# Optimization experiments

Measured on AMD Instinct MI355X. Metric: run time of the kernel, lower is better.

The kernel has to match this reference:

```python
import jax, jax.numpy as jnp
import numpy as np
import math

B, S, E, H = 2, 2048, 1024, 16
D = E // H  # head dim = 64


def setup_inputs() -> dict:
    key = jax.random.key(0)
    ks = jax.random.split(key, 7)
    scale = 1.0 / math.sqrt(E)
    return {
        "query": jax.random.normal(ks[0], (B, S, E), dtype=jnp.float32),
        "key": jax.random.normal(ks[1], (B, S, E), dtype=jnp.float32),
        "value": jax.random.normal(ks[2], (B, S, E), dtype=jnp.float32),
        # packed in-projection: (3E, E) weights, (3E,) bias, q/k/v order
        "in_proj_weight": jax.random.normal(ks[3], (3 * E, E), dtype=jnp.float32) * scale,
        "in_proj_bias": jnp.zeros((3 * E,), dtype=jnp.float32),
        "out_proj_weight": jax.random.normal(ks[4], (E, E), dtype=jnp.float32) * scale,
        "out_proj_bias": jnp.zeros((E,), dtype=jnp.float32),
    }


def reference(query, key, value, in_proj_weight, in_proj_bias, out_proj_weight, out_proj_bias):
    # packed in-projection (q, k, v order), F.linear convention: x @ W^T + b
    w_q, w_k, w_v = jnp.split(in_proj_weight, 3, axis=0)
    b_q, b_k, b_v = jnp.split(in_proj_bias, 3, axis=0)
    q = query @ w_q.T + b_q   # [B, S, E]
    k = key @ w_k.T + b_k
    v = value @ w_v.T + b_v

    # split heads: [B, S, E] -> [B, H, S, D]
    def heads(x):
        return x.reshape(B, S, H, D).transpose(0, 2, 1, 3)

    q, k, v = heads(q), heads(k), heads(v)
    q = q / jnp.asarray(math.sqrt(D), dtype=q.dtype)

    # naive softmax attention (materializes [B, H, S, S] as original bmm+softmax+bmm)
    scores = jnp.einsum("bhqd,bhkd->bhqk", q, k)
    attn = jax.nn.softmax(scores, axis=-1)
    out = jnp.einsum("bhqk,bhkd->bhqd", attn, v)  # [B, H, S, D]

    out = out.transpose(0, 2, 1, 3).reshape(B, S, E)
    return out @ out_proj_weight.T + out_proj_bias
```

## Files before the change

### kernel.cpp

```cpp
#include <hip/hip_runtime.h>
#include <stdint.h>

#define LOG2E 1.44269504088896340736f

typedef __bf16 bf16x8 __attribute__((ext_vector_type(8)));
typedef float f32x4 __attribute__((ext_vector_type(4)));
typedef float f32x16 __attribute__((ext_vector_type(16)));

static constexpr int Bb = 2, Ss = 2048, Ee = 1024, Hh = 16, Dd = 64;
static constexpr int BSE = Bb * Ss * Ee;

static constexpr size_t OFF_QB    = 0;
static constexpr size_t OFF_KB    = 4194304;
static constexpr size_t OFF_VB    = 8388608;
static constexpr size_t OFF_WQKV  = 12582912;
static constexpr size_t OFF_WOUT  = 15728640;
static constexpr size_t OFF_QH    = 16777216;
static constexpr size_t OFF_KH    = 20971520;
static constexpr size_t OFF_VH    = 25165824;
static constexpr size_t OFF_OB    = 29360128;

__device__ __forceinline__ uint16_t f32_bf16(float f) {
    uint32_t u = __builtin_bit_cast(uint32_t, f);
    u += 0x7fffu + ((u >> 16) & 1u);
    return (uint16_t)(u >> 16);
}

__device__ __forceinline__ uint32_t cvt_pk_bf16(float a, float b) {
    uint32_t r;
    asm("v_cvt_pk_bf16_f32 %0, %1, %2" : "=v"(r) : "v"(a), "v"(b));
    return r;
}

__device__ __forceinline__ void perm32swap(uint32_t& x, uint32_t& y) {
    asm("v_permlane32_swap_b32 %0, %1" : "+v"(x), "+v"(y));
}

__global__ __launch_bounds__(256) void cvt_kernel(
    const float* __restrict__ q, const float* __restrict__ k, const float* __restrict__ v,
    const float* __restrict__ w1, uint16_t* __restrict__ ws)
{
    const float* srcs[4] = {q, k, v, w1};
    const int ns4[4] = {BSE/4, BSE/4, BSE/4, (3*Ee*Ee)/4};
    uint16_t* dsts[4] = {ws+OFF_QB, ws+OFF_KB, ws+OFF_VB, ws+OFF_WQKV};
    int z = blockIdx.z;
    int i = blockIdx.x * blockDim.x + threadIdx.x;
    if (i < ns4[z]) {
        float4 f = ((const float4*)srcs[z])[i];
        ushort4 o;
        o.x = f32_bf16(f.x); o.y = f32_bf16(f.y);
        o.z = f32_bf16(f.z); o.w = f32_bf16(f.w);
        ((ushort4*)dsts[z])[i] = o;
    }
}

__global__ __launch_bounds__(256) void cvt_one(
    const float* __restrict__ src, uint16_t* __restrict__ dst)
{
    int i = blockIdx.x * 256 + threadIdx.x;
    float4 f = ((const float4*)src)[i];
    ushort4 o;
    o.x = f32_bf16(f.x); o.y = f32_bf16(f.y);
    o.z = f32_bf16(f.z); o.w = f32_bf16(f.w);
    ((ushort4*)dst)[i] = o;
}

template<int MODE>
__global__ __launch_bounds__(256) void gemm_nt(
    const uint16_t* __restrict__ Aq, const uint16_t* __restrict__ Ak,
    const uint16_t* __restrict__ Av, const uint16_t* __restrict__ Bw,
    const float* __restrict__ bias, uint16_t* __restrict__ OutB,
    float* __restrict__ OutF)
{
    constexpr int K = Ee, N = Ee;
    const int tid = threadIdx.x;
    const int l = tid & 63, w = tid >> 6;
    const int wr = w >> 1, wc = w & 1;
    const int tm = blockIdx.y, tn = blockIdx.x;
    const int z = (MODE == 0) ? blockIdx.z : 0;

    const uint16_t* A = (MODE == 0) ? (z == 0 ? Aq : (z == 1 ? Ak : Av)) : Aq;
    const uint16_t* Bp = Bw + (size_t)z * Ee * Ee;
    const float* bp = bias + (size_t)z * Ee;

    __shared__ alignas(16) uint16_t As[128 * 32];
    __shared__ alignas(16) uint16_t Bs[128 * 32];

    f32x4 acc[4][4] = {};
    const int arow = tm * 128;
    const int bcol = tn * 128;

    for (int kt = 0; kt < K / 32; ++kt) {
        __syncthreads();
        #pragma unroll
        for (int it = 0; it < 2; ++it) {
            int c = tid + it * 256;
            int row = c >> 2, qq = c & 3;
            const uint16_t* ga = A  + (size_t)(arow + row) * K + kt * 32 + qq * 8;
            const uint16_t* gb = Bp + (size_t)(bcol + row) * K + kt * 32 + qq * 8;
            __builtin_amdgcn_global_load_lds(
                (const __attribute__((address_space(1))) void*)ga,
                (__attribute__((address_space(3))) void*)(As + c * 8), 16, 0, 0);
            __builtin_amdgcn_global_load_lds(
                (const __attribute__((address_space(1))) void*)gb,
                (__attribute__((address_space(3))) void*)(Bs + c * 8), 16, 0, 0);
        }
        __syncthreads();
        bf16x8 aF[4], bF[4];
        #pragma unroll
        for (int m = 0; m < 4; ++m)
            aF[m] = *(const bf16x8*)(As + ((wr * 64 + m * 16 + (l & 15)) * 32 + (l >> 4) * 8));
        #pragma unroll
        for (int n = 0; n < 4; ++n)
            bF[n] = *(const bf16x8*)(Bs + ((wc * 64 + n * 16 + (l & 15)) * 32 + (l >> 4) * 8));
        #pragma unroll
        for (int m = 0; m < 4; ++m)
            #pragma unroll
            for (int n = 0; n < 4; ++n)
                acc[m][n] = __builtin_amdgcn_mfma_f32_16x16x32_bf16(aF[m], bF[n], acc[m][n], 0, 0, 0);
    }

    #pragma unroll
    for (int n = 0; n < 4; ++n) {
        int col = bcol + wc * 64 + n * 16 + (l & 15);
        float bn = bp[col];
        #pragma unroll
        for (int m = 0; m < 4; ++m) {
            int row0 = arow + wr * 64 + m * 16 + (l >> 4) * 4;
            #pragma unroll
            for (int j = 0; j < 4; ++j) {
                int row = row0 + j;
                float v = acc[m][n][j] + bn;
                if (MODE == 0) {
                    if (z == 0) v *= 0.125f * LOG2E;
                    int b = row >> 11, s = row & 2047, hh = col >> 6, d = col & 63;
                    OutB[(size_t)z * BSE + (size_t)(((b * Hh) + hh) * Ss + s) * Dd + d] = f32_bf16(v);
                } else {
                    OutF[(size_t)row * N + col] = v;
                }
            }
        }
    }
}

__global__ __launch_bounds__(256, 3) void attn_kernel(
    const uint16_t* __restrict__ Qh, const uint16_t* __restrict__ Kh,
    const uint16_t* __restrict__ Vh, float* __restrict__ po,
    float* __restrict__ lpart)
{
    const int tid = threadIdx.x;
    const int l = tid & 63, w = tid >> 6;
    const int q = l & 31, hi = l >> 5;

    const int orig = blockIdx.x;
    const int L = (orig & 7) * 128 + (orig >> 3);
    const int qb = L & 15, split = (L >> 4) & 1, bh = L >> 5;

    const int q0 = qb * 128;
    const int keyb = split * 1024;
    const size_t base = (size_t)bh * Ss * Dd;

    __shared__ alignas(16) uint16_t Ks[2][64 * 64];
    __shared__ alignas(16) uint16_t Vt[2][64 * 64];

    bf16x8 qf[4];
    {
        const uint16_t* qp = Qh + base + (size_t)(q0 + w * 32 + q) * Dd + hi * 8;
        #pragma unroll
        for (int m = 0; m < 4; ++m) qf[m] = *(const bf16x8*)(qp + 16 * m);
    }

    const int kp = tid >> 3, c8v = tid & 7;
    uint4 vg0, vg1;

    auto loadK_lds = [&](int key0, int buf) {
        #pragma unroll
        for (int it = 0; it < 2; ++it) {
            int c = tid + 256 * it, row = c >> 3, cc = c & 7;
            const uint16_t* gk = Kh + base + (size_t)(key0 + row) * Dd + ((cc ^ (row & 7)) * 8);
            __builtin_amdgcn_global_load_lds(
                (const __attribute__((address_space(1))) void*)gk,
                (__attribute__((address_space(3))) void*)(&Ks[buf][c * 8]), 16, 0, 0);
        }
    };
    auto loadV = [&](int key0) {
        vg0 = *(const uint4*)(Vh + base + (size_t)(key0 + 2 * kp) * Dd + c8v * 8);
        vg1 = *(const uint4*)(Vh + base + (size_t)(key0 + 2 * kp + 1) * Dd + c8v * 8);
    };

    loadK_lds(keyb, 0);
    loadV(keyb);

    f32x16 o0 = {}, o1 = {};
    float lsum = 0.f;

    auto build_pb = [&](const f32x16& sv, bf16x8* pbout) {
        uint32_t W[4][2];
        #pragma unroll
        for (int a = 0; a < 4; ++a) {
            float p0 = __builtin_amdgcn_exp2f(sv[4 * a + 0]);
            float p1 = __builtin_amdgcn_exp2f(sv[4 * a + 1]);
            float p2 = __builtin_amdgcn_exp2f(sv[4 * a + 2]);
            float p3 = __builtin_amdgcn_exp2f(sv[4 * a + 3]);
            lsum += (p0 + p1) + (p2 + p3);
            W[a][0] = cvt_pk_bf16(p0, p1);
            W[a][1] = cvt_pk_bf16(p2, p3);
        }
        #pragma unroll
        for (int kl = 0; kl < 2; ++kl) {
            uint32_t x0 = W[2 * kl][0], x1 = W[2 * kl][1];
            uint32_t y0 = W[2 * kl + 1][0], y1 = W[2 * kl + 1][1];
            perm32swap(x0, y0);
            perm32swap(x1, y1);
            union { uint32_t u[4]; bf16x8 v; } pu;
            pu.u[0] = x0; pu.u[1] = x1; pu.u[2] = y0; pu.u[3] = y1;
            pbout[kl] = pu.v;
        }
    };

    #pragma unroll 2
    for (int kt = 0; kt < 16; ++kt) {
        const int b = kt & 1;
        __syncthreads();

        {
            const uint16_t* e0 = (const uint16_t*)&vg0;
            const uint16_t* e1 = (const uint16_t*)&vg1;
            #pragma unroll
            for (int e = 0; e < 8; ++e) {
                int d = c8v * 8 + e;
                int swz = (kp >> 2) ^ e ^ c8v;
                uint32_t pk2 = (uint32_t)e0[e] | ((uint32_t)e1[e] << 16);
                *(uint32_t*)&Vt[b][d * 64 + swz * 8 + ((2 * kp) & 7)] = pk2;
            }
        }

        if (kt < 15) {
            loadK_lds(keyb + (kt + 1) * 64, b ^ 1);
            loadV(keyb + (kt + 1) * 64);
        }

        __syncthreads();

        f32x16 s0 = {}, s1 = {};
        __builtin_amdgcn_s_setprio(1);
        #pragma unroll
        for (int m = 0; m < 4; ++m) {
            int sw = ((2 * m + hi) ^ (q & 7)) << 3;
            bf16x8 k0 = *(const bf16x8*)&Ks[b][q * 64 + sw];
            bf16x8 k1 = *(const bf16x8*)&Ks[b][(32 + q) * 64 + sw];
            s0 = __builtin_amdgcn_mfma_f32_32x32x16_bf16(k0, qf[m], s0, 0, 0, 0);
            s1 = __builtin_amdgcn_mfma_f32_32x32x16_bf16(k1, qf[m], s1, 0, 0, 0);
        }
        __builtin_amdgcn_s_setprio(0);

        bf16x8 pb[4];
        build_pb(s0, pb + 0);
        build_pb(s1, pb + 2);

        __builtin_amdgcn_s_setprio(1);
        #pragma unroll
        for (int ka = 0; ka < 4; ++ka) {
            #pragma unroll
            for (int dt = 0; dt < 2; ++dt) {
                int d = 32 * dt + q;
                int swz = (2 * ka + hi) ^ (d & 7) ^ (d >> 3);
                bf16x8 vf = *(const bf16x8*)&Vt[b][d * 64 + swz * 8];
                if (dt == 0)
                    o0 = __builtin_amdgcn_mfma_f32_32x32x16_bf16(vf, pb[ka], o0, 0, 0, 0);
                else
                    o1 = __builtin_amdgcn_mfma_f32_32x32x16_bf16(vf, pb[ka], o1, 0, 0, 0);
            }
        }
        __builtin_amdgcn_s_setprio(0);
    }

    float lr = lsum + __shfl_xor(lsum, 32);
    const int qrow = q0 + w * 32 + q;
    const int sb = split * 32 + bh;
    if (hi == 0) lpart[(size_t)sb * 2048 + qrow] = lr;
    #pragma unroll
    for (int dt = 0; dt < 2; ++dt) {
        const f32x16& oo = dt ? o1 : o0;
        #pragma unroll
        for (int rr = 0; rr < 16; ++rr) {
            int d = 32 * dt + (rr & 3) + 8 * (rr >> 2) + 4 * hi;
            po[((size_t)sb * 64 + d) * 2048 + qrow] = oo[rr];
        }
    }
}

__global__ __launch_bounds__(256) void combine_kernel(
    const float* __restrict__ po, const float* __restrict__ lp,
    uint16_t* __restrict__ Ob)
{
    __shared__ float T[64][65];
    const int t = threadIdx.x;
    const int bh = blockIdx.y;
    const int q0 = blockIdx.x * 64;
    const int qq = t & 63;
    const float inv = 1.0f / (lp[bh * 2048 + q0 + qq] + lp[(32 + bh) * 2048 + q0 + qq]);
    const size_t b0 = (size_t)bh * 64 * 2048;
    const size_t b1 = (size_t)(32 + bh) * 64 * 2048;
    #pragma unroll
    for (int i = 0; i < 16; ++i) {
        int d = i * 4 + (t >> 6);
        size_t off = (size_t)d * 2048 + q0 + qq;
        T[d][qq] = (po[b0 + off] + po[b1 + off]) * inv;
    }
    __syncthreads();
    const int row = t >> 2, dc = (t & 3) * 16;
    const int bb = bh >> 4, hh = bh & 15;
    union { uint16_t u[16]; uint4 v[2]; } pk;
    #pragma unroll
    for (int e = 0; e < 16; ++e) pk.u[e] = f32_bf16(T[dc + e][row]);
    uint16_t* dst = &Ob[(size_t)(bb * 2048 + q0 + row) * 1024 + hh * 64 + dc];
    *(uint4*)dst = pk.v[0];
    *((uint4*)dst + 1) = pk.v[1];
}

extern "C" void kernel_launch(void* const* d_in, const int* in_sizes, int n_in,
                              void* d_out, int out_size, void* d_ws, size_t ws_size,
                              hipStream_t stream) {
    (void)in_sizes; (void)n_in; (void)out_size; (void)ws_size;
    const float* query = (const float*)d_in[0];
    const float* key   = (const float*)d_in[1];
    const float* value = (const float*)d_in[2];
    const float* w_in  = (const float*)d_in[3];
    const float* b_in  = (const float*)d_in[4];
    const float* w_out = (const float*)d_in[5];
    const float* b_out = (const float*)d_in[6];
    uint16_t* ws = (uint16_t*)d_ws;

    uint16_t* qb    = ws + OFF_QB;
    uint16_t* kb    = ws + OFF_KB;
    uint16_t* vb    = ws + OFF_VB;
    uint16_t* wqkvb = ws + OFF_WQKV;
    uint16_t* woutb = ws + OFF_WOUT;
    uint16_t* Qh    = ws + OFF_QH;
    uint16_t* Kh    = ws + OFF_KH;
    uint16_t* Vh    = ws + OFF_VH;
    uint16_t* Ob    = ws + OFF_OB;
    float*    po    = (float*)d_ws;
    float*    lpart = (float*)d_out;

    cvt_kernel<<<dim3(4096, 1, 4), 256, 0, stream>>>(query, key, value, w_in, ws);
    gemm_nt<0><<<dim3(8, 32, 3), 256, 0, stream>>>(qb, kb, vb, wqkvb, b_in, Qh, nullptr);
    attn_kernel<<<dim3(1024), 256, 0, stream>>>(Qh, Kh, Vh, po, lpart);
    combine_kernel<<<dim3(32, 32), 256, 0, stream>>>(po, lpart, Ob);
    cvt_one<<<dim3(1024), 256, 0, stream>>>(w_out, woutb);
    gemm_nt<1><<<dim3(8, 32, 1), 256, 0, stream>>>(Ob, nullptr, nullptr, woutb, b_out, nullptr, (float*)d_out);
}
```

Before: 138.3 us.

## Emit V transposed from projection GEMM and process two query tiles per attention block

The V projection is computed as W_v·V^T, so the GEMM writes V directly in a [bh, d, s] transposed layout. The attention kernel can then stage V into LDS with async global_load_lds instead of loading it through registers and transposing it in software. This also drops one barrier per iteration. Each attention block now covers 256 queries (two 128-row sets sharing every K/V tile), halving the grid and the K/V traffic per query, at the cost of more registers and lower occupancy (launch bound 2).

```diff
diff --git a/kernel.cpp b/kernel.cpp
--- a/kernel.cpp
+++ b/kernel.cpp
@@ -76,11 +76,13 @@
     const int tid = threadIdx.x;
     const int l = tid & 63, w = tid >> 6;
     const int wr = w >> 1, wc = w & 1;
-    const int tm = blockIdx.y, tn = blockIdx.x;
     const int z = (MODE == 0) ? blockIdx.z : 0;
-
-    const uint16_t* A = (MODE == 0) ? (z == 0 ? Aq : (z == 1 ? Ak : Av)) : Aq;
-    const uint16_t* Bp = Bw + (size_t)z * Ee * Ee;
+    const bool VT = (MODE == 0) && (z == 2);
+    const int tm = VT ? blockIdx.x : blockIdx.y;
+    const int tn = VT ? blockIdx.y : blockIdx.x;
+
+    const uint16_t* A = (MODE == 0) ? (z == 0 ? Aq : (z == 1 ? Ak : Bw + 2 * Ee * Ee)) : Aq;
+    const uint16_t* Bp = VT ? Av : (Bw + (size_t)z * Ee * Ee);
     const float* bp = bias + (size_t)z * Ee;
 
     __shared__ alignas(16) uint16_t As[128 * 32];
@@ -123,29 +125,35 @@
     #pragma unroll
     for (int n = 0; n < 4; ++n) {
         int col = bcol + wc * 64 + n * 16 + (l & 15);
-        float bn = bp[col];
+        float bn = VT ? 0.f : bp[col];
         #pragma unroll
         for (int m = 0; m < 4; ++m) {
             int row0 = arow + wr * 64 + m * 16 + (l >> 4) * 4;
             #pragma unroll
             for (int j = 0; j < 4; ++j) {
                 int row = row0 + j;
-                float v = acc[m][n][j] + bn;
                 if (MODE == 0) {
-                    if (z == 0) v *= 0.125f * LOG2E;
-                    int b = row >> 11, s = row & 2047, hh = col >> 6, d = col & 63;
-                    OutB[(size_t)z * BSE + (size_t)(((b * Hh) + hh) * Ss + s) * Dd + d] = f32_bf16(v);
+                    if (VT) {
+                        float v = acc[m][n][j] + bp[row];
+                        int hh = row >> 6, d = row & 63, b = col >> 11, s = col & 2047;
+                        OutB[2 * (size_t)BSE + ((size_t)((b * Hh + hh) * Dd + d)) * Ss + s] = f32_bf16(v);
+                    } else {
+                        float v = acc[m][n][j] + bn;
+                        if (z == 0) v *= 0.125f * LOG2E;
+                        int b = row >> 11, s = row & 2047, hh = col >> 6, d = col & 63;
+                        OutB[(size_t)z * BSE + (size_t)(((b * Hh) + hh) * Ss + s) * Dd + d] = f32_bf16(v);
+                    }
                 } else {
-                    OutF[(size_t)row * N + col] = v;
+                    OutF[(size_t)row * N + col] = acc[m][n][j] + bn;
                 }
             }
         }
     }
 }
 
-__global__ __launch_bounds__(256, 3) void attn_kernel(
+__global__ __launch_bounds__(256, 2) void attn_kernel(
     const uint16_t* __restrict__ Qh, const uint16_t* __restrict__ Kh,
-    const uint16_t* __restrict__ Vh, float* __restrict__ po,
+    const uint16_t* __restrict__ Vtg, float* __restrict__ po,
     float* __restrict__ lpart)
 {
     const int tid = threadIdx.x;
@@ -153,48 +161,53 @@
     const int q = l & 31, hi = l >> 5;
 
     const int orig = blockIdx.x;
-    const int L = (orig & 7) * 128 + (orig >> 3);
-    const int qb = L & 15, split = (L >> 4) & 1, bh = L >> 5;
-
-    const int q0 = qb * 128;
+    const int L = (orig & 7) * 64 + (orig >> 3);
+    const int qb = L & 7, split = (L >> 3) & 1, bh = L >> 4;
+
+    const int q0 = qb * 256;
     const int keyb = split * 1024;
-    const size_t base = (size_t)bh * Ss * Dd;
+    const size_t baseK = (size_t)bh * Ss * Dd;
+    const size_t baseV = (size_t)bh * Dd * Ss;
 
     __shared__ alignas(16) uint16_t Ks[2][64 * 64];
     __shared__ alignas(16) uint16_t Vt[2][64 * 64];
 
-    bf16x8 qf[4];
+    bf16x8 qfA[4], qfB[4];
     {
-        const uint16_t* qp = Qh + base + (size_t)(q0 + w * 32 + q) * Dd + hi * 8;
-        #pragma unroll
-        for (int m = 0; m < 4; ++m) qf[m] = *(const bf16x8*)(qp + 16 * m);
-    }
-
-    const int kp = tid >> 3, c8v = tid & 7;
-    uint4 vg0, vg1;
-
-    auto loadK_lds = [&](int key0, int buf) {
+        const uint16_t* qp = Qh + baseK + (size_t)(q0 + w * 32 + q) * Dd + hi * 8;
+        #pragma unroll
+        for (int m = 0; m < 4; ++m) {
+            qfA[m] = *(const bf16x8*)(qp + 16 * m);
+            qfB[m] = *(const bf16x8*)(qp + 128 * Dd + 16 * m);
+        }
+    }
+
+    auto stage = [&](int kt, int buf) {
+        const int key0 = keyb + kt * 64;
         #pragma unroll
         for (int it = 0; it < 2; ++it) {
             int c = tid + 256 * it, row = c >> 3, cc = c & 7;
-            const uint16_t* gk = Kh + base + (size_t)(key0 + row) * Dd + ((cc ^ (row & 7)) * 8);
+            const uint16_t* gk = Kh + baseK + (size_t)(key0 + row) * Dd + ((cc ^ (row & 7)) * 8);
             __builtin_amdgcn_global_load_lds(
                 (const __attribute__((address_space(1))) void*)gk,
                 (__attribute__((address_space(3))) void*)(&Ks[buf][c * 8]), 16, 0, 0);
         }
+        #pragma unroll
+        for (int it = 0; it < 2; ++it) {
+            int c = tid + 256 * it, d = c >> 3, j = c & 7;
+            const uint16_t* gv = Vtg + baseV + (size_t)d * Ss + key0 + 8 * (j ^ (d & 7) ^ (d >> 3));
+            __builtin_amdgcn_global_load_lds(
+                (const __attribute__((address_space(1))) void*)gv,
+                (__attribute__((address_space(3))) void*)(&Vt[buf][c * 8]), 16, 0, 0);
+        }
     };
-    auto loadV = [&](int key0) {
-        vg0 = *(const uint4*)(Vh + base + (size_t)(key0 + 2 * kp) * Dd + c8v * 8);
-        vg1 = *(const uint4*)(Vh + base + (size_t)(key0 + 2 * kp + 1) * Dd + c8v * 8);
-    };
-
-    loadK_lds(keyb, 0);
-    loadV(keyb);
-
-    f32x16 o0 = {}, o1 = {};
-    float lsum = 0.f;
-
-    auto build_pb = [&](const f32x16& sv, bf16x8* pbout) {
+
+    stage(0, 0);
+
+    f32x16 oA0 = {}, oA1 = {}, oB0 = {}, oB1 = {};
+    float lsumA = 0.f, lsumB = 0.f;
+
+    auto build_pb = [&](const f32x16& sv, bf16x8* pbout, float& lsum) {
         uint32_t W[4][2];
         #pragma unroll
         for (int a = 0; a < 4; ++a) {
@@ -223,69 +236,83 @@
         const int b = kt & 1;
         __syncthreads();
 
+        if (kt < 15) stage(kt + 1, b ^ 1);
+
         {
-            const uint16_t* e0 = (const uint16_t*)&vg0;
-            const uint16_t* e1 = (const uint16_t*)&vg1;
-            #pragma unroll
-            for (int e = 0; e < 8; ++e) {
-                int d = c8v * 8 + e;
-                int swz = (kp >> 2) ^ e ^ c8v;
-                uint32_t pk2 = (uint32_t)e0[e] | ((uint32_t)e1[e] << 16);
-                *(uint32_t*)&Vt[b][d * 64 + swz * 8 + ((2 * kp) & 7)] = pk2;
+            f32x16 s0 = {}, s1 = {};
+            __builtin_amdgcn_s_setprio(1);
+            #pragma unroll
+            for (int m = 0; m < 4; ++m) {
+                int sw = ((2 * m + hi) ^ (q & 7)) << 3;
+                bf16x8 k0 = *(const bf16x8*)&Ks[b][q * 64 + sw];
+                bf16x8 k1 = *(const bf16x8*)&Ks[b][(32 + q) * 64 + sw];
+                s0 = __builtin_amdgcn_mfma_f32_32x32x16_bf16(k0, qfA[m], s0, 0, 0, 0);
+                s1 = __builtin_amdgcn_mfma_f32_32x32x16_bf16(k1, qfA[m], s1, 0, 0, 0);
             }
-        }
-
-        if (kt < 15) {
-            loadK_lds(keyb + (kt + 1) * 64, b ^ 1);
-            loadV(keyb + (kt + 1) * 64);
-        }
-
-        __syncthreads();
-
-        f32x16 s0 = {}, s1 = {};
-        __builtin_amdgcn_s_setprio(1);
-        #pragma unroll
-        for (int m = 0; m < 4; ++m) {
-            int sw = ((2 * m + hi) ^ (q & 7)) << 3;
-            bf16x8 k0 = *(const bf16x8*)&Ks[b][q * 64 + sw];
-            bf16x8 k1 = *(const bf16x8*)&Ks[b][(32 + q) * 64 + sw];
-            s0 = __builtin_amdgcn_mfma_f32_32x32x16_bf16(k0, qf[m], s0, 0, 0, 0);
-            s1 = __builtin_amdgcn_mfma_f32_32x32x16_bf16(k1, qf[m], s1, 0, 0, 0);
-        }
-        __builtin_amdgcn_s_setprio(0);
-
-        bf16x8 pb[4];
-        build_pb(s0, pb + 0);
-        build_pb(s1, pb + 2);
-
-        __builtin_amdgcn_s_setprio(1);
-        #pragma unroll
-        for (int ka = 0; ka < 4; ++ka) {
-            #pragma unroll
-            for (int dt = 0; dt < 2; ++dt) {
-                int d = 32 * dt + q;
-                int swz = (2 * ka + hi) ^ (d & 7) ^ (d >> 3);
-                bf16x8 vf = *(const bf16x8*)&Vt[b][d * 64 + swz * 8];
-                if (dt == 0)
-                    o0 = __builtin_amdgcn_mfma_f32_32x32x16_bf16(vf, pb[ka], o0, 0, 0, 0);
-                else
-                    o1 = __builtin_amdgcn_mfma_f32_32x32x16_bf16(vf, pb[ka], o1, 0, 0, 0);
+            __builtin_amdgcn_s_setprio(0);
+            bf16x8 pb[4];
+            build_pb(s0, pb + 0, lsumA);
+            build_pb(s1, pb + 2, lsumA);
+            __builtin_amdgcn_s_setprio(1);
+            #pragma unroll
+            for (int ka = 0; ka < 4; ++ka)
+                #pragma unroll
+                for (int dt = 0; dt < 2; ++dt) {
+                    int d = 32 * dt + q;
+                    int swz = (2 * ka + hi) ^ (d & 7) ^ (d >> 3);
+                    bf16x8 vf = *(const bf16x8*)&Vt[b][d * 64 + swz * 8];
+                    if (dt == 0) oA0 = __builtin_amdgcn_mfma_f32_32x32x16_bf16(vf, pb[ka], oA0, 0, 0, 0);
+                    else         oA1 = __builtin_amdgcn_mfma_f32_32x32x16_bf16(vf, pb[ka], oA1, 0, 0, 0);
+                }
+            __builtin_amdgcn_s_setprio(0);
+        }
+        {
+            f32x16 s0 = {}, s1 = {};
+            __builtin_amdgcn_s_setprio(1);
+            #pragma unroll
+            for (int m = 0; m < 4; ++m) {
+                int sw = ((2 * m + hi) ^ (q & 7)) << 3;
+                bf16x8 k0 = *(const bf16x8*)&Ks[b][q * 64 + sw];
+                bf16x8 k1 = *(const bf16x8*)&Ks[b][(32 + q) * 64 + sw];
+                s0 = __builtin_amdgcn_mfma_f32_32x32x16_bf16(k0, qfB[m], s0, 0, 0, 0);
+                s1 = __builtin_amdgcn_mfma_f32_32x32x16_bf16(k1, qfB[m], s1, 0, 0, 0);
             }
-        }
-        __builtin_amdgcn_s_setprio(0);
-    }
-
-    float lr = lsum + __shfl_xor(lsum, 32);
-    const int qrow = q0 + w * 32 + q;
+            __builtin_amdgcn_s_setprio(0);
+            bf16x8 pb[4];
+            build_pb(s0, pb + 0, lsumB);
+            build_pb(s1, pb + 2, lsumB);
+            __builtin_amdgcn_s_setprio(1);
+            #pragma unroll
+            for (int ka = 0; ka < 4; ++ka)
+                #pragma unroll
+                for (int dt = 0; dt < 2; ++dt) {
+                    int d = 32 * dt + q;
+                    int swz = (2 * ka + hi) ^ (d & 7) ^ (d >> 3);
+                    bf16x8 vf = *(const bf16x8*)&Vt[b][d * 64 + swz * 8];
+                    if (dt == 0) oB0 = __builtin_amdgcn_mfma_f32_32x32x16_bf16(vf, pb[ka], oB0, 0, 0, 0);
+                    else         oB1 = __builtin_amdgcn_mfma_f32_32x32x16_bf16(vf, pb[ka], oB1, 0, 0, 0);
+                }
+            __builtin_amdgcn_s_setprio(0);
+        }
+    }
+
     const int sb = split * 32 + bh;
-    if (hi == 0) lpart[(size_t)sb * 2048 + qrow] = lr;
+    const int qrowA = q0 + w * 32 + q, qrowB = qrowA + 128;
+    float lrA = lsumA + __shfl_xor(lsumA, 32);
+    float lrB = lsumB + __shfl_xor(lsumB, 32);
+    if (hi == 0) {
+        lpart[(size_t)sb * 2048 + qrowA] = lrA;
+        lpart[(size_t)sb * 2048 + qrowB] = lrB;
+    }
     #pragma unroll
     for (int dt = 0; dt < 2; ++dt) {
-        const f32x16& oo = dt ? o1 : o0;
+        const f32x16& ooA = dt ? oA1 : oA0;
+        const f32x16& ooB = dt ? oB1 : oB0;
         #pragma unroll
         for (int rr = 0; rr < 16; ++rr) {
             int d = 32 * dt + (rr & 3) + 8 * (rr >> 2) + 4 * hi;
-            po[((size_t)sb * 64 + d) * 2048 + qrow] = oo[rr];
+            po[((size_t)sb * 64 + d) * 2048 + qrowA] = ooA[rr];
+            po[((size_t)sb * 64 + d) * 2048 + qrowB] = ooB[rr];
         }
     }
 }
@@ -339,14 +366,14 @@
     uint16_t* woutb = ws + OFF_WOUT;
     uint16_t* Qh    = ws + OFF_QH;
     uint16_t* Kh    = ws + OFF_KH;
-    uint16_t* Vh    = ws + OFF_VH;
+    uint16_t* Vtg   = ws + OFF_VH;
     uint16_t* Ob    = ws + OFF_OB;
     float*    po    = (float*)d_ws;
     float*    lpart = (float*)d_out;
 
     cvt_kernel<<<dim3(4096, 1, 4), 256, 0, stream>>>(query, key, value, w_in, ws);
     gemm_nt<0><<<dim3(8, 32, 3), 256, 0, stream>>>(qb, kb, vb, wqkvb, b_in, Qh, nullptr);
-    attn_kernel<<<dim3(1024), 256, 0, stream>>>(Qh, Kh, Vh, po, lpart);
+    attn_kernel<<<dim3(512), 256, 0, stream>>>(Qh, Kh, Vtg, po, lpart);
     combine_kernel<<<dim3(32, 32), 256, 0, stream>>>(po, lpart, Ob);
     cvt_one<<<dim3(1024), 256, 0, stream>>>(w_out, woutb);
     gemm_nt<1><<<dim3(8, 32, 1), 256, 0, stream>>>(Ob, nullptr, nullptr, woutb, b_out, nullptr, (float*)d_out);
```

After: 180.2 us. 30.3% more time.

## Produce transposed V from projection GEMM and async-load it in attention

Applied to the files above, without the earlier changes.

The V projection is recomputed as W_v times value^T, so the QKV GEMM writes V directly in a [b,h,d,s] layout. The attention kernel can then stage V^T into LDS with swizzled global_load_lds, the same way it stages K. This removes the per-tile register shuffle that transposed V, plus one of the two barriers in each key-tile iteration. In exchange, the GEMM gets a separate, differently indexed epilogue for the V slice, and the attention loop now relies on the top-of-loop barrier to make the async LDS loads visible before they are read.

```diff
diff --git a/kernel.cpp b/kernel.cpp
--- a/kernel.cpp
+++ b/kernel.cpp
@@ -76,11 +76,13 @@
     const int tid = threadIdx.x;
     const int l = tid & 63, w = tid >> 6;
     const int wr = w >> 1, wc = w & 1;
-    const int tm = blockIdx.y, tn = blockIdx.x;
     const int z = (MODE == 0) ? blockIdx.z : 0;
-
-    const uint16_t* A = (MODE == 0) ? (z == 0 ? Aq : (z == 1 ? Ak : Av)) : Aq;
-    const uint16_t* Bp = Bw + (size_t)z * Ee * Ee;
+    const bool VT = (MODE == 0) && (z == 2);
+    const int tm = VT ? blockIdx.x : blockIdx.y;
+    const int tn = VT ? blockIdx.y : blockIdx.x;
+
+    const uint16_t* A = (MODE == 0) ? (z == 0 ? Aq : (z == 1 ? Ak : Bw + 2 * Ee * Ee)) : Aq;
+    const uint16_t* Bp = VT ? Av : (Bw + (size_t)z * Ee * Ee);
     const float* bp = bias + (size_t)z * Ee;
 
     __shared__ alignas(16) uint16_t As[128 * 32];
@@ -123,20 +125,26 @@
     #pragma unroll
     for (int n = 0; n < 4; ++n) {
         int col = bcol + wc * 64 + n * 16 + (l & 15);
-        float bn = bp[col];
+        float bn = VT ? 0.f : bp[col];
         #pragma unroll
         for (int m = 0; m < 4; ++m) {
             int row0 = arow + wr * 64 + m * 16 + (l >> 4) * 4;
             #pragma unroll
             for (int j = 0; j < 4; ++j) {
                 int row = row0 + j;
-                float v = acc[m][n][j] + bn;
                 if (MODE == 0) {
-                    if (z == 0) v *= 0.125f * LOG2E;
-                    int b = row >> 11, s = row & 2047, hh = col >> 6, d = col & 63;
-                    OutB[(size_t)z * BSE + (size_t)(((b * Hh) + hh) * Ss + s) * Dd + d] = f32_bf16(v);
+                    if (VT) {
+                        float v = acc[m][n][j] + bp[row];
+                        int hh = row >> 6, d = row & 63, b = col >> 11, s = col & 2047;
+                        OutB[2 * (size_t)BSE + ((size_t)((b * Hh + hh) * Dd + d)) * Ss + s] = f32_bf16(v);
+                    } else {
+                        float v = acc[m][n][j] + bn;
+                        if (z == 0) v *= 0.125f * LOG2E;
+                        int b = row >> 11, s = row & 2047, hh = col >> 6, d = col & 63;
+                        OutB[(size_t)z * BSE + (size_t)(((b * Hh) + hh) * Ss + s) * Dd + d] = f32_bf16(v);
+                    }
                 } else {
-                    OutF[(size_t)row * N + col] = v;
+                    OutF[(size_t)row * N + col] = acc[m][n][j] + bn;
                 }
             }
         }
@@ -145,7 +153,7 @@
 
 __global__ __launch_bounds__(256, 3) void attn_kernel(
     const uint16_t* __restrict__ Qh, const uint16_t* __restrict__ Kh,
-    const uint16_t* __restrict__ Vh, float* __restrict__ po,
+    const uint16_t* __restrict__ Vtg, float* __restrict__ po,
     float* __restrict__ lpart)
 {
     const int tid = threadIdx.x;
@@ -158,38 +166,40 @@
 
     const int q0 = qb * 128;
     const int keyb = split * 1024;
-    const size_t base = (size_t)bh * Ss * Dd;
+    const size_t baseK = (size_t)bh * Ss * Dd;
+    const size_t baseV = (size_t)bh * Dd * Ss;
 
     __shared__ alignas(16) uint16_t Ks[2][64 * 64];
     __shared__ alignas(16) uint16_t Vt[2][64 * 64];
 
     bf16x8 qf[4];
     {
-        const uint16_t* qp = Qh + base + (size_t)(q0 + w * 32 + q) * Dd + hi * 8;
+        const uint16_t* qp = Qh + baseK + (size_t)(q0 + w * 32 + q) * Dd + hi * 8;
         #pragma unroll
         for (int m = 0; m < 4; ++m) qf[m] = *(const bf16x8*)(qp + 16 * m);
     }
 
-    const int kp = tid >> 3, c8v = tid & 7;
-    uint4 vg0, vg1;
-
-    auto loadK_lds = [&](int key0, int buf) {
+    auto stage = [&](int kt, int buf) {
+        const int key0 = keyb + kt * 64;
         #pragma unroll
         for (int it = 0; it < 2; ++it) {
             int c = tid + 256 * it, row = c >> 3, cc = c & 7;
-            const uint16_t* gk = Kh + base + (size_t)(key0 + row) * Dd + ((cc ^ (row & 7)) * 8);
+            const uint16_t* gk = Kh + baseK + (size_t)(key0 + row) * Dd + ((cc ^ (row & 7)) * 8);
             __builtin_amdgcn_global_load_lds(
                 (const __attribute__((address_space(1))) void*)gk,
                 (__attribute__((address_space(3))) void*)(&Ks[buf][c * 8]), 16, 0, 0);
         }
+        #pragma unroll
+        for (int it = 0; it < 2; ++it) {
+            int c = tid + 256 * it, d = c >> 3, j = c & 7;
+            const uint16_t* gv = Vtg + baseV + (size_t)d * Ss + key0 + 8 * (j ^ (d & 7) ^ (d >> 3));
+            __builtin_amdgcn_global_load_lds(
+                (const __attribute__((address_space(1))) void*)gv,
+                (__attribute__((address_space(3))) void*)(&Vt[buf][c * 8]), 16, 0, 0);
+        }
     };
-    auto loadV = [&](int key0) {
-        vg0 = *(const uint4*)(Vh + base + (size_t)(key0 + 2 * kp) * Dd + c8v * 8);
-        vg1 = *(const uint4*)(Vh + base + (size_t)(key0 + 2 * kp + 1) * Dd + c8v * 8);
-    };
-
-    loadK_lds(keyb, 0);
-    loadV(keyb);
+
+    stage(0, 0);
 
     f32x16 o0 = {}, o1 = {};
     float lsum = 0.f;
@@ -223,24 +233,7 @@
         const int b = kt & 1;
         __syncthreads();
 
-        {
-            const uint16_t* e0 = (const uint16_t*)&vg0;
-            const uint16_t* e1 = (const uint16_t*)&vg1;
-            #pragma unroll
-            for (int e = 0; e < 8; ++e) {
-                int d = c8v * 8 + e;
-                int swz = (kp >> 2) ^ e ^ c8v;
-                uint32_t pk2 = (uint32_t)e0[e] | ((uint32_t)e1[e] << 16);
-                *(uint32_t*)&Vt[b][d * 64 + swz * 8 + ((2 * kp) & 7)] = pk2;
-            }
-        }
-
-        if (kt < 15) {
-            loadK_lds(keyb + (kt + 1) * 64, b ^ 1);
-            loadV(keyb + (kt + 1) * 64);
-        }
-
-        __syncthreads();
+        if (kt < 15) stage(kt + 1, b ^ 1);
 
         f32x16 s0 = {}, s1 = {};
         __builtin_amdgcn_s_setprio(1);
@@ -339,14 +332,14 @@
     uint16_t* woutb = ws + OFF_WOUT;
     uint16_t* Qh    = ws + OFF_QH;
     uint16_t* Kh    = ws + OFF_KH;
-    uint16_t* Vh    = ws + OFF_VH;
+    uint16_t* Vtg   = ws + OFF_VH;
     uint16_t* Ob    = ws + OFF_OB;
     float*    po    = (float*)d_ws;
     float*    lpart = (float*)d_out;
 
     cvt_kernel<<<dim3(4096, 1, 4), 256, 0, stream>>>(query, key, value, w_in, ws);
     gemm_nt<0><<<dim3(8, 32, 3), 256, 0, stream>>>(qb, kb, vb, wqkvb, b_in, Qh, nullptr);
-    attn_kernel<<<dim3(1024), 256, 0, stream>>>(Qh, Kh, Vh, po, lpart);
+    attn_kernel<<<dim3(1024), 256, 0, stream>>>(Qh, Kh, Vtg, po, lpart);
     combine_kernel<<<dim3(32, 32), 256, 0, stream>>>(po, lpart, Ob);
     cvt_one<<<dim3(1024), 256, 0, stream>>>(w_out, woutb);
     gemm_nt<1><<<dim3(8, 32, 1), 256, 0, stream>>>(Ob, nullptr, nullptr, woutb, b_out, nullptr, (float*)d_out);
```

After: 164.0 us. 1.19x slower.
